# Optimization experiments

Measured on AMD Instinct MI355X. Metric: run time of the kernel, lower is better.

Reference implementation:

```python
import jax, jax.numpy as jnp
import numpy as np

COST_CLASS, COST_BBOX, COST_GIOU = 1.0, 1.0, 1.0
ALPHA, GAMMA, EPS = 0.25, 2.0, 1e-8


def box_cxcywh_to_xyxy(b):
    cx, cy, w, h = b[..., 0], b[..., 1], b[..., 2], b[..., 3]
    return jnp.stack([cx - 0.5 * w, cy - 0.5 * h, cx + 0.5 * w, cy + 0.5 * h], axis=-1)


def pairwise_generalized_box_iou(b1, b2):
    # b1: [N,4], b2: [M,4] in xyxy -> [N,M]
    area1 = (b1[:, 2] - b1[:, 0]) * (b1[:, 3] - b1[:, 1])
    area2 = (b2[:, 2] - b2[:, 0]) * (b2[:, 3] - b2[:, 1])
    lt = jnp.maximum(b1[:, None, :2], b2[None, :, :2])
    rb = jnp.minimum(b1[:, None, 2:], b2[None, :, 2:])
    wh = jnp.clip(rb - lt, 0.0)
    inter = wh[..., 0] * wh[..., 1]
    union = area1[:, None] + area2[None, :] - inter
    iou = inter / union
    lt_c = jnp.minimum(b1[:, None, :2], b2[None, :, :2])
    rb_c = jnp.maximum(b1[:, None, 2:], b2[None, :, 2:])
    wh_c = jnp.clip(rb_c - lt_c, 0.0)
    area_c = wh_c[..., 0] * wh_c[..., 1]
    return iou - (area_c - union) / area_c


def setup_inputs() -> dict:
    key = jax.random.key(0)
    k1, k2, k3, k4 = jax.random.split(key, 4)
    bs, nq, nc, T = 8, 900, 91, 200
    pred_logits = jax.random.normal(k1, (bs, nq, nc), dtype=jnp.float32)
    pred_boxes = jax.random.uniform(k2, (bs, nq, 4), dtype=jnp.float32)
    tgt_boxes = jax.random.uniform(k3, (bs, T, 4), dtype=jnp.float32)
    tgt_ids = jax.random.randint(k4, (bs, T), 0, nc)
    return {"pred_logits": pred_logits, "pred_boxes": pred_boxes,
            "tgt_boxes": tgt_boxes, "tgt_ids": tgt_ids}


def reference(pred_logits, pred_boxes, tgt_boxes, tgt_ids):
    bs, nq, nc = pred_logits.shape
    T = tgt_boxes.shape[1]
    out_prob = jax.nn.sigmoid(pred_logits.reshape(bs * nq, nc))   # [BQ, C]
    out_bbox = pred_boxes.reshape(bs * nq, 4)                     # [BQ, 4]
    ids = tgt_ids.reshape(-1)                                     # [BT]
    tb = tgt_boxes.reshape(-1, 4)                                 # [BT, 4]

    # focal classification cost
    neg_cost = (1.0 - ALPHA) * out_prob ** GAMMA * -jnp.log(1.0 - out_prob + EPS)
    pos_cost = ALPHA * (1.0 - out_prob) ** GAMMA * -jnp.log(out_prob + EPS)
    cost_class = (pos_cost - neg_cost)[:, ids]                    # [BQ, BT]

    # L1 bbox cost (cdist p=1)
    cost_bbox = jnp.sum(jnp.abs(out_bbox[:, None, :] - tb[None, :, :]), axis=-1)

    # GIoU cost
    cost_giou = -pairwise_generalized_box_iou(box_cxcywh_to_xyxy(out_bbox),
                                              box_cxcywh_to_xyxy(tb))

    C = COST_BBOX * cost_bbox + COST_CLASS * cost_class + COST_GIOU * cost_giou
    C = C.reshape(bs, nq, bs * T)

    # per-batch diagonal block: C[i, :, i*T:(i+1)*T], then argmin over queries
    C4 = C.reshape(bs, nq, bs, T)
    b = jnp.arange(bs)
    blocks = C4[b, :, b, :]                                       # [bs, nq, T]
    idx_i = jnp.argmin(blocks, axis=1).astype(jnp.int64)          # [bs, T]
    return C, idx_i
```

## Files before the change

### kernel.cpp

```cpp
#include <hip/hip_runtime.h>

#define BS 8
#define NQ 900
#define NC 91
#define TT 200
#define NT (BS*TT)
#define NROWS (BS*NQ)
#define RPB 4
#define C_ELEMS ((size_t)NROWS*(size_t)NT)

__global__ __launch_bounds__(256) void cost_kernel(
    const float* __restrict__ logits,
    const float4* __restrict__ pboxes,
    const float4* __restrict__ tboxes,
    const int*   __restrict__ tids,
    float* __restrict__ C)
{
    __shared__ float cls[RPB][NC];
    __shared__ float pb[RPB][8];
    const int row0 = blockIdx.x * RPB;
    const int tid  = threadIdx.x;

    for (int i = tid; i < RPB * NC; i += 256) {
        const int r = i / NC, c = i - r * NC;
        const float x = logits[(size_t)(row0 + r) * NC + c];
        const float p = 1.0f / (1.0f + expf(-x));
        const float pos = 0.25f * (1.0f - p) * (1.0f - p) * (-logf(p + 1e-8f));
        const float neg = 0.75f * p * p * (-logf(1.0f - p + 1e-8f));
        cls[r][c] = pos - neg;
    }
    if (tid < RPB) {
        const float4 b = pboxes[row0 + tid];
        pb[tid][0] = b.x; pb[tid][1] = b.y; pb[tid][2] = b.z; pb[tid][3] = b.w;
        pb[tid][4] = b.x - 0.5f * b.z; pb[tid][5] = b.y - 0.5f * b.w;
        pb[tid][6] = b.x + 0.5f * b.z; pb[tid][7] = b.y + 0.5f * b.w;
    }
    __syncthreads();

    for (int c4 = tid; c4 < NT / 4; c4 += 256) {
        float4 tb[4]; int id[4];
        float tx1[4], ty1[4], tx2[4], ty2[4], ta[4];
        #pragma unroll
        for (int k = 0; k < 4; ++k) {
            tb[k] = tboxes[c4 * 4 + k];
            id[k] = tids[c4 * 4 + k];
            tx1[k] = tb[k].x - 0.5f * tb[k].z; ty1[k] = tb[k].y - 0.5f * tb[k].w;
            tx2[k] = tb[k].x + 0.5f * tb[k].z; ty2[k] = tb[k].y + 0.5f * tb[k].w;
            ta[k] = (tx2[k] - tx1[k]) * (ty2[k] - ty1[k]);
        }
        #pragma unroll
        for (int r = 0; r < RPB; ++r) {
            const float cx = pb[r][0], cy = pb[r][1], w = pb[r][2], h = pb[r][3];
            const float px1 = pb[r][4], py1 = pb[r][5], px2 = pb[r][6], py2 = pb[r][7];
            const float pa = (px2 - px1) * (py2 - py1);
            float res[4];
            #pragma unroll
            for (int k = 0; k < 4; ++k) {
                const float l1 = fabsf(cx - tb[k].x) + fabsf(cy - tb[k].y)
                               + fabsf(w  - tb[k].z) + fabsf(h  - tb[k].w);
                const float ltx = fmaxf(px1, tx1[k]), lty = fmaxf(py1, ty1[k]);
                const float rbx = fminf(px2, tx2[k]), rby = fminf(py2, ty2[k]);
                const float iw = fmaxf(rbx - ltx, 0.0f), ih = fmaxf(rby - lty, 0.0f);
                const float inter = iw * ih;
                const float uni = pa + ta[k] - inter;
                const float iou = inter / uni;
                const float cltx = fminf(px1, tx1[k]), clty = fminf(py1, ty1[k]);
                const float crbx = fmaxf(px2, tx2[k]), crby = fmaxf(py2, ty2[k]);
                const float cw = fmaxf(crbx - cltx, 0.0f), ch = fmaxf(crby - clty, 0.0f);
                const float ac = cw * ch;
                const float giou = iou - (ac - uni) / ac;
                res[k] = l1 + cls[r][id[k]] - giou;
            }
            float4 out; out.x = res[0]; out.y = res[1]; out.z = res[2]; out.w = res[3];
            reinterpret_cast<float4*>(C)[(size_t)(row0 + r) * (NT / 4) + c4] = out;
        }
    }
}

__device__ __forceinline__ unsigned long long packkey(float v, int q) {
    unsigned u = __float_as_uint(v);
    u = (u & 0x80000000u) ? ~u : (u | 0x80000000u);
    return ((unsigned long long)u << 32) | (unsigned)q;
}

__global__ __launch_bounds__(64) void argmin_kernel(
    const float* __restrict__ C, float* __restrict__ out, int tail_elems)
{
    const int i = blockIdx.x;
    const int b = i / TT;
    const int lane = threadIdx.x;
    const float* base = C + (size_t)b * NQ * NT + (size_t)b * TT + (i - b * TT);
    unsigned long long best = ~0ull;
    for (int q = lane; q < NQ; q += 64) {
        const unsigned long long pk = packkey(base[(size_t)q * NT], q);
        best = best < pk ? best : pk;
    }
    #pragma unroll
    for (int off = 32; off > 0; off >>= 1) {
        const unsigned long long o = __shfl_down(best, off, 64);
        best = best < o ? best : o;
    }
    if (lane == 0) {
        const unsigned q = (unsigned)(best & 0xffffffffu);
        float* tail = out + C_ELEMS;
        if (tail_elems >= 3200) {
            reinterpret_cast<long long*>(tail)[i] = (long long)q;
        } else if (tail_elems >= 1600) {
            tail[i] = (float)q;
        }
    }
}

extern "C" void kernel_launch(void* const* d_in, const int* in_sizes, int n_in,
                              void* d_out, int out_size, void* d_ws, size_t ws_size,
                              hipStream_t stream) {
    const float*  logits = (const float*)d_in[0];
    const float4* pboxes = (const float4*)d_in[1];
    const float4* tboxes = (const float4*)d_in[2];
    const int*    tids   = (const int*)d_in[3];
    float* C = (float*)d_out;
    (void)d_ws; (void)ws_size;

    cost_kernel<<<NROWS / RPB, 256, 0, stream>>>(logits, pboxes, tboxes, tids, C);
    const int tail = out_size - (int)C_ELEMS;
    argmin_kernel<<<BS * TT, 64, 0, stream>>>(C, C, tail);
}
```

Measured before the change: 110.0 us.

## Fuse per-batch argmin into cost kernel via 64-bit atomicMin slots

Folds the per-batch argmin over queries into the cost kernel. Each thread keeps a packed value/index minimum for its diagonal-block columns and commits it with 64-bit atomicMin into workspace slots, so the second pass that re-read strided columns of C is gone. Small init and finalize kernels are added. It also doubles rows per block to 8 and replaces the IEEE divisions with rcp plus one Newton step, which can change the low bits of C and the tie-breaking of the argmin.

```diff
diff --git a/kernel.cpp b/kernel.cpp
--- a/kernel.cpp
+++ b/kernel.cpp
@@ -6,15 +6,33 @@
 #define TT 200
 #define NT (BS*TT)
 #define NROWS (BS*NQ)
-#define RPB 4
+#define RPB 8
+#define NBLK (NROWS/RPB)
 #define C_ELEMS ((size_t)NROWS*(size_t)NT)
 
-__global__ __launch_bounds__(256) void cost_kernel(
+__device__ __forceinline__ float fastrcp(float x) {
+    float r = __builtin_amdgcn_rcpf(x);
+    return r * fmaf(-x, r, 2.0f);
+}
+
+__device__ __forceinline__ unsigned long long packkey(float v, int q) {
+    unsigned u = __float_as_uint(v);
+    u = (u & 0x80000000u) ? ~u : (u | 0x80000000u);
+    return ((unsigned long long)u << 32) | (unsigned)q;
+}
+
+__global__ void init_slots(unsigned long long* __restrict__ slots) {
+    const int i = blockIdx.x * blockDim.x + threadIdx.x;
+    if (i < NT) slots[i] = ~0ull;
+}
+
+__global__ __launch_bounds__(256) void cost_argmin_kernel(
     const float* __restrict__ logits,
     const float4* __restrict__ pboxes,
     const float4* __restrict__ tboxes,
     const int*   __restrict__ tids,
-    float* __restrict__ C)
+    float* __restrict__ C,
+    unsigned long long* __restrict__ slots)
 {
     __shared__ float cls[RPB][NC];
     __shared__ float pb[RPB][8];
@@ -38,21 +56,32 @@
     __syncthreads();
 
     for (int c4 = tid; c4 < NT / 4; c4 += 256) {
-        float4 tb[4]; int id[4];
+        float4 tb[4];
         float tx1[4], ty1[4], tx2[4], ty2[4], ta[4];
+        float clsv[4];
         #pragma unroll
         for (int k = 0; k < 4; ++k) {
             tb[k] = tboxes[c4 * 4 + k];
-            id[k] = tids[c4 * 4 + k];
             tx1[k] = tb[k].x - 0.5f * tb[k].z; ty1[k] = tb[k].y - 0.5f * tb[k].w;
             tx2[k] = tb[k].x + 0.5f * tb[k].z; ty2[k] = tb[k].y + 0.5f * tb[k].w;
             ta[k] = (tx2[k] - tx1[k]) * (ty2[k] - ty1[k]);
         }
+        int id[4];
+        #pragma unroll
+        for (int k = 0; k < 4; ++k) id[k] = tids[c4 * 4 + k];
+
+        const int cdiv = c4 / 50;
+        unsigned long long mk[4] = {~0ull, ~0ull, ~0ull, ~0ull};
+        bool any = false;
+
         #pragma unroll
         for (int r = 0; r < RPB; ++r) {
+            const int grow = row0 + r;
             const float cx = pb[r][0], cy = pb[r][1], w = pb[r][2], h = pb[r][3];
             const float px1 = pb[r][4], py1 = pb[r][5], px2 = pb[r][6], py2 = pb[r][7];
             const float pa = (px2 - px1) * (py2 - py1);
+            #pragma unroll
+            for (int k = 0; k < 4; ++k) clsv[k] = cls[r][id[k]];
             float res[4];
             #pragma unroll
             for (int k = 0; k < 4; ++k) {
@@ -63,51 +92,45 @@
                 const float iw = fmaxf(rbx - ltx, 0.0f), ih = fmaxf(rby - lty, 0.0f);
                 const float inter = iw * ih;
                 const float uni = pa + ta[k] - inter;
-                const float iou = inter / uni;
                 const float cltx = fminf(px1, tx1[k]), clty = fminf(py1, ty1[k]);
                 const float crbx = fmaxf(px2, tx2[k]), crby = fmaxf(py2, ty2[k]);
                 const float cw = fmaxf(crbx - cltx, 0.0f), ch = fmaxf(crby - clty, 0.0f);
                 const float ac = cw * ch;
-                const float giou = iou - (ac - uni) / ac;
-                res[k] = l1 + cls[r][id[k]] - giou;
+                const float giou = inter * fastrcp(uni) - (ac - uni) * fastrcp(ac);
+                res[k] = l1 + clsv[k] - giou;
             }
             float4 out; out.x = res[0]; out.y = res[1]; out.z = res[2]; out.w = res[3];
-            reinterpret_cast<float4*>(C)[(size_t)(row0 + r) * (NT / 4) + c4] = out;
+            reinterpret_cast<float4*>(C)[(size_t)grow * (NT / 4) + c4] = out;
+
+            const int brow = grow / NQ;
+            if (brow == cdiv) {
+                const int q = grow - brow * NQ;
+                any = true;
+                #pragma unroll
+                for (int k = 0; k < 4; ++k) {
+                    const unsigned long long pk = packkey(res[k], q);
+                    mk[k] = mk[k] < pk ? mk[k] : pk;
+                }
+            }
+        }
+        if (any) {
+            #pragma unroll
+            for (int k = 0; k < 4; ++k)
+                atomicMin(&slots[c4 * 4 + k], mk[k]);
         }
     }
 }
 
-__device__ __forceinline__ unsigned long long packkey(float v, int q) {
-    unsigned u = __float_as_uint(v);
-    u = (u & 0x80000000u) ? ~u : (u | 0x80000000u);
-    return ((unsigned long long)u << 32) | (unsigned)q;
-}
-
-__global__ __launch_bounds__(64) void argmin_kernel(
-    const float* __restrict__ C, float* __restrict__ out, int tail_elems)
-{
-    const int i = blockIdx.x;
-    const int b = i / TT;
-    const int lane = threadIdx.x;
-    const float* base = C + (size_t)b * NQ * NT + (size_t)b * TT + (i - b * TT);
-    unsigned long long best = ~0ull;
-    for (int q = lane; q < NQ; q += 64) {
-        const unsigned long long pk = packkey(base[(size_t)q * NT], q);
-        best = best < pk ? best : pk;
-    }
-    #pragma unroll
-    for (int off = 32; off > 0; off >>= 1) {
-        const unsigned long long o = __shfl_down(best, off, 64);
-        best = best < o ? best : o;
-    }
-    if (lane == 0) {
-        const unsigned q = (unsigned)(best & 0xffffffffu);
-        float* tail = out + C_ELEMS;
-        if (tail_elems >= 3200) {
-            reinterpret_cast<long long*>(tail)[i] = (long long)q;
-        } else if (tail_elems >= 1600) {
-            tail[i] = (float)q;
-        }
+__global__ void write_idx(const unsigned long long* __restrict__ slots,
+                          float* __restrict__ out, int tail_elems) {
+    const int i = blockIdx.x * blockDim.x + threadIdx.x;
+    if (i >= NT) return;
+    const unsigned q = (unsigned)(slots[i] & 0xffffffffu);
+    float* tail = out + C_ELEMS;
+    if (tail_elems >= 3200) {
+        reinterpret_cast<long long*>(tail)[i] = (long long)q;
+    } else if (tail_elems >= 1600) {
+        tail[i] = (float)q;
     }
 }
 
@@ -119,9 +142,10 @@
     const float4* tboxes = (const float4*)d_in[2];
     const int*    tids   = (const int*)d_in[3];
     float* C = (float*)d_out;
-    (void)d_ws; (void)ws_size;
+    unsigned long long* slots = (unsigned long long*)d_ws;
 
-    cost_kernel<<<NROWS / RPB, 256, 0, stream>>>(logits, pboxes, tboxes, tids, C);
+    init_slots<<<(NT + 255) / 256, 256, 0, stream>>>(slots);
+    cost_argmin_kernel<<<NBLK, 256, 0, stream>>>(logits, pboxes, tboxes, tids, C, slots);
     const int tail = out_size - (int)C_ELEMS;
-    argmin_kernel<<<BS * TT, 64, 0, stream>>>(C, C, tail);
+    write_idx<<<(NT + 255) / 256, 256, 0, stream>>>(slots, C, tail);
 }
```

After: 104.2 us. 1.06x faster.
